# Kernel tuning notes

Measured on AMD Instinct MI355X. Metric: run time of the kernel, lower is better.

## Reference

```python
import jax, jax.numpy as jnp
import numpy as np

HEADS = 12
IDX = 0


def setup_inputs() -> dict:
    key = jax.random.key(0)
    ks = jax.random.split(key, 6)
    B, H, W, C = 16, 64, 64, 384
    x = jax.random.normal(ks[0], (B, H * W, C), dtype=jnp.float32)
    qkv_w = jax.random.normal(ks[1], (3 * C, C), dtype=jnp.float32) * 0.02
    proj_w = jax.random.normal(ks[2], (C, C), dtype=jnp.float32) * 0.02
    proj_b = jax.random.normal(ks[3], (C,), dtype=jnp.float32) * 0.02
    lepe_w = jax.random.normal(ks[4], (C, 1, 3, 3), dtype=jnp.float32) * 0.02  # depthwise, torch OIHW with I=1
    lepe_b = jax.random.normal(ks[5], (C,), dtype=jnp.float32) * 0.02
    return {"x": x, "qkv_w": qkv_w, "proj_w": proj_w, "proj_b": proj_b,
            "lepe_w": lepe_w, "lepe_b": lepe_b, "H": H, "W": W}


def _lepe_forward(x, qkv_w, proj_w, proj_b, lepe_w, lepe_b, H, W):
    B, N, C = x.shape
    hd = C // HEADS
    scale = hd ** (-0.5)
    x_img = x.reshape(B, H, W, C)

    if IDX == 0:
        # vertical strips: attend over H within each column
        x_split = jnp.transpose(x_img, (0, 2, 1, 3)).reshape(B * W, H, C)
    else:
        x_split = x_img.reshape(B * H, W, C)
    S, L, _ = x_split.shape

    qkv = (x_split @ qkv_w.T).reshape(S, L, 3, HEADS, hd)
    qkv = jnp.transpose(qkv, (2, 0, 3, 1, 4))  # (3, S, heads, L, hd)
    q, k, v = qkv[0], qkv[1], qkv[2]

    attn = jnp.einsum('shld,shmd->shlm', q, k) * scale
    attn = jax.nn.softmax(attn, axis=-1)
    out = jnp.einsum('shlm,shmd->shld', attn, v)           # (S, heads, L, hd)
    out = jnp.transpose(out, (0, 2, 1, 3)).reshape(S, L, C)
    # faithful to torch: view(B, out_H, out_W, C).view(B, H*W, C) -- no permute back for idx==0
    out_flat = out.reshape(B, H * W, C)

    # depthwise 3x3 conv LePE on the original (H, W) layout
    lepe = jax.lax.conv_general_dilated(
        jnp.transpose(x_img, (0, 3, 1, 2)), lepe_w,
        window_strides=(1, 1), padding='SAME',
        feature_group_count=C,
        dimension_numbers=('NCHW', 'OIHW', 'NCHW'))
    lepe = lepe + lepe_b[None, :, None, None]
    lepe = jnp.transpose(lepe, (0, 2, 3, 1)).reshape(B, H * W, C)

    return (out_flat + lepe) @ proj_w.T + proj_b


def reference(x, qkv_w, proj_w, proj_b, lepe_w, lepe_b, H, W):
    return _lepe_forward(x, qkv_w, proj_w, proj_b, lepe_w, lepe_b, H, W)
```

## Files before the change

### kernel.cpp

```cpp
#include <hip/hip_runtime.h>


typedef _Float16 f16;
typedef _Float16 f16x8 __attribute__((ext_vector_type(8)));
typedef float    f32x4 __attribute__((ext_vector_type(4)));

__device__ __forceinline__ f32x4 mfma_16x16x32(f16x8 a, f16x8 b, f32x4 c) {
  return __builtin_amdgcn_mfma_f32_16x16x32_f16(a, b, c, 0, 0, 0);
}

__device__ __forceinline__ void gl_lds16(const f16* g, f16* l) {
  __builtin_amdgcn_global_load_lds((const __attribute__((address_space(1))) void*)g,
                                   (__attribute__((address_space(3))) void*)l, 16, 0, 0);
}

__global__ __launch_bounds__(256) void k_cvt(const float* __restrict__ src,
                                             f16* __restrict__ dst, int n8) {
  int i = blockIdx.x * 256 + threadIdx.x;
  if (i >= n8) return;
  const f32x4* s4 = (const f32x4*)src;
  f32x4 a = s4[2 * i], b = s4[2 * i + 1];
  f16x8 o;
#pragma unroll
  for (int j = 0; j < 4; ++j) { o[j] = (f16)a[j]; o[4 + j] = (f16)b[j]; }
  *(f16x8*)&dst[(long)i * 8] = o;
}

__global__ __launch_bounds__(256) void k_prep(const float* __restrict__ x,
                                              const float* __restrict__ lw,
                                              const float* __restrict__ lb,
                                              f16* __restrict__ x16,
                                              f16* __restrict__ lepe16) {
  __shared__ float ws[9 * 384];
  __shared__ float bs[384];
  for (int i = threadIdx.x; i < 3456; i += 256) {
    int c = i / 9, tap = i - c * 9;
    ws[tap * 384 + (c & 7) * 48 + (c >> 3)] = lw[i];
  }
  for (int i = threadIdx.x; i < 384; i += 256)
    bs[(i & 7) * 48 + (i >> 3)] = lb[i];
  __syncthreads();

  int chunk = blockIdx.x * 256 + threadIdx.x;
  int token = chunk / 48;
  int c0 = (chunk - token * 48) * 8;
  int cg = c0 >> 3;
  int b = token >> 12, n = token & 4095, h = n >> 6, w = n & 63;
  const float* xb = x + (long)(b << 12) * 384;

  float a8[8];
#pragma unroll
  for (int cc = 0; cc < 8; ++cc) a8[cc] = bs[cc * 48 + cg];
  f16x8 cv;
#pragma unroll
  for (int ky = 0; ky < 3; ++ky) {
    int hh = h + ky - 1;
    if (hh < 0 || hh > 63) continue;
#pragma unroll
    for (int kx = 0; kx < 3; ++kx) {
      int ww = w + kx - 1;
      if (ww < 0 || ww > 63) continue;
      const float* p = xb + (long)((hh << 6) + ww) * 384 + c0;
      float4 u = *(const float4*)p;
      float4 v = *(const float4*)(p + 4);
      float xs[8] = {u.x, u.y, u.z, u.w, v.x, v.y, v.z, v.w};
      if (ky == 1 && kx == 1) {
#pragma unroll
        for (int cc = 0; cc < 8; ++cc) cv[cc] = (f16)xs[cc];
      }
      int tap = ky * 3 + kx;
#pragma unroll
      for (int cc = 0; cc < 8; ++cc)
        a8[cc] += xs[cc] * ws[tap * 384 + cc * 48 + cg];
    }
  }
  f16x8 o;
#pragma unroll
  for (int cc = 0; cc < 8; ++cc) o[cc] = (f16)a8[cc];
  *(f16x8*)&x16[(long)token * 384 + c0] = cv;
  *(f16x8*)&lepe16[(long)token * 384 + c0] = o;
}

__global__ __launch_bounds__(256) void k_qkv(const f16* __restrict__ A,
                                             const f16* __restrict__ Bt,
                                             f16* __restrict__ C) {
  __shared__ alignas(16) f16 smem[2 * 128 * 64];
  f16* As = smem;
  f16* Bs = smem + 128 * 64;
  f16* buf = smem;
  const int tid = threadIdx.x;
  const int lane = tid & 63;
  const int wave = tid >> 6;
  const int wr = wave >> 1, wc = wave & 1;
  const int ln = lane & 15, quad = lane >> 4;
  const int bid = blockIdx.x;
  const int xcd = bid & 7;
  const int s = bid >> 3;
  const int mq = s / 9;
  const int mt = xcd * 64 + mq;
  const int nt = s - mq * 9;
  const long m0 = (long)mt * 128;
  const int n0 = nt * 128;

  f32x4 acc[4][4] = {};
  for (int k0 = 0; k0 < 384; k0 += 64) {
#pragma unroll
    for (int r = 0; r < 4; ++r) {
      int flat = r * 256 + tid;
      int row = flat >> 3, c8 = flat & 7;
      int sc8 = (c8 ^ (row & 7)) * 8;
      gl_lds16(&A[(m0 + row) * 384 + k0 + sc8], &As[flat * 8]);
      gl_lds16(&Bt[(long)(n0 + row) * 384 + k0 + sc8], &Bs[flat * 8]);
    }
    __syncthreads();
#pragma unroll
    for (int ks = 0; ks < 2; ++ks) {
      f16x8 a[4], b[4];
#pragma unroll
      for (int i = 0; i < 4; ++i)
        a[i] = *(const f16x8*)&As[(wr * 64 + i * 16 + ln) * 64 +
                                  ((ks * 4 + quad) ^ (ln & 7)) * 8];
#pragma unroll
      for (int j = 0; j < 4; ++j)
        b[j] = *(const f16x8*)&Bs[(wc * 64 + j * 16 + ln) * 64 +
                                  ((ks * 4 + quad) ^ (ln & 7)) * 8];
#pragma unroll
      for (int i = 0; i < 4; ++i)
#pragma unroll
        for (int j = 0; j < 4; ++j)
          acc[i][j] = mfma_16x16x32(a[i], b[j], acc[i][j]);
    }
    __syncthreads();
  }

  for (int half = 0; half < 2; ++half) {
    __syncthreads();
    if (wr == half) {
#pragma unroll
      for (int i = 0; i < 4; ++i)
#pragma unroll
        for (int j = 0; j < 4; ++j)
#pragma unroll
          for (int r = 0; r < 4; ++r)
            buf[(i * 16 + quad * 4 + r) * 136 + wc * 64 + j * 16 + ln] =
                (f16)acc[i][j][r];
    }
    __syncthreads();
#pragma unroll
    for (int it = 0; it < 4; ++it) {
      int flat = it * 256 + tid;
      int row = flat >> 4;
      int c8 = flat & 15;
      int t = (int)m0 + half * 64 + row;
      int nn = t & 4095;
      long prow = (long)(t & ~4095) + ((nn & 63) << 6) + (nn >> 6);
      *(f16x8*)&C[prow * 1152 + n0 + c8 * 8] =
          *(const f16x8*)&buf[row * 136 + c8 * 8];
    }
  }
}

__global__ __launch_bounds__(256) void k_attn(const f16* __restrict__ qkv,
                                              f16* __restrict__ attnout) {
  __shared__ alignas(16) f16 shp[4][7424];
  const int lane = threadIdx.x & 63;
  const int wave = threadIdx.x >> 6;
  const int ln = lane & 15, quad = lane >> 4, q8 = quad * 8;
  const int b = blockIdx.x >> 6, w = blockIdx.x & 63;
  const long sbase = (long)b * 4096 + (long)w * 64;

  f16* qs = shp[wave];
  f16* ks = shp[wave] + 2560;
  f16* vt = shp[wave] + 5120;
  f16* ps = shp[wave];
  f16* obuf = shp[wave];
  const float qscale = 0.17677669529663687f;

  for (int hi = 0; hi < 3; ++hi) {
    const int hh = wave * 3 + hi;
#pragma unroll
    for (int r = 0; r < 4; ++r) {
      int flat = r * 64 + lane;
      int l = flat >> 2, dg = (flat & 3) * 8;
      long ta = (sbase + l) * 1152 + hh * 32 + dg;
      f16x8 qv = *(const f16x8*)&qkv[ta];
      f16x8 kv = *(const f16x8*)&qkv[ta + 384];
      f16x8 vv = *(const f16x8*)&qkv[ta + 768];
#pragma unroll
      for (int ii = 0; ii < 8; ++ii) qv[ii] = (f16)((float)qv[ii] * qscale);
      *(f16x8*)&qs[l * 40 + dg] = qv;
      *(f16x8*)&ks[l * 40 + dg] = kv;
#pragma unroll
      for (int ii = 0; ii < 8; ++ii) vt[(dg + ii) * 72 + l] = vv[ii];
    }
    f16x8 aq[4], bk[4];
#pragma unroll
    for (int i = 0; i < 4; ++i) aq[i] = *(const f16x8*)&qs[(i * 16 + ln) * 40 + q8];
#pragma unroll
    for (int j = 0; j < 4; ++j) bk[j] = *(const f16x8*)&ks[(j * 16 + ln) * 40 + q8];
    f32x4 sc[4][4] = {};
#pragma unroll
    for (int i = 0; i < 4; ++i)
#pragma unroll
      for (int j = 0; j < 4; ++j) sc[i][j] = mfma_16x16x32(aq[i], bk[j], sc[i][j]);

    float rs[4][4];
#pragma unroll
    for (int i = 0; i < 4; ++i)
#pragma unroll
      for (int r = 0; r < 4; ++r) {
        float m = -1e30f;
#pragma unroll
        for (int j = 0; j < 4; ++j) m = fmaxf(m, sc[i][j][r]);
#pragma unroll
        for (int off = 1; off < 16; off <<= 1) m = fmaxf(m, __shfl_xor(m, off, 64));
        float sum = 0.f;
#pragma unroll
        for (int j = 0; j < 4; ++j) {
          float p = __expf(sc[i][j][r] - m);
          sc[i][j][r] = p;
          sum += p;
        }
#pragma unroll
        for (int off = 1; off < 16; off <<= 1) sum += __shfl_xor(sum, off, 64);
        rs[i][r] = 1.0f / sum;
      }

#pragma unroll
    for (int i = 0; i < 4; ++i)
#pragma unroll
      for (int j = 0; j < 4; ++j)
#pragma unroll
        for (int r = 0; r < 4; ++r)
          ps[(i * 16 + quad * 4 + r) * 72 + j * 16 + ln] = (f16)sc[i][j][r];

    f32x4 oc[4][2] = {};
#pragma unroll
    for (int k2 = 0; k2 < 2; ++k2) {
      f16x8 ap[4], bv[2];
#pragma unroll
      for (int i = 0; i < 4; ++i)
        ap[i] = *(const f16x8*)&ps[(i * 16 + ln) * 72 + k2 * 32 + q8];
#pragma unroll
      for (int j = 0; j < 2; ++j)
        bv[j] = *(const f16x8*)&vt[(j * 16 + ln) * 72 + k2 * 32 + q8];
#pragma unroll
      for (int i = 0; i < 4; ++i)
#pragma unroll
        for (int j = 0; j < 2; ++j) oc[i][j] = mfma_16x16x32(ap[i], bv[j], oc[i][j]);
    }

#pragma unroll
    for (int i = 0; i < 4; ++i)
#pragma unroll
      for (int j = 0; j < 2; ++j)
#pragma unroll
        for (int r = 0; r < 4; ++r)
          obuf[(i * 16 + quad * 4 + r) * 40 + j * 16 + ln] =
              (f16)(oc[i][j][r] * rs[i][r]);
    {
      int row = lane >> 1, hf = lane & 1;
#pragma unroll
      for (int rr = 0; rr < 2; ++rr) {
        int rw = rr * 32 + row;
        const f16* ob = &obuf[rw * 40 + hf * 16];
        f16x8 o0 = *(const f16x8*)ob;
        f16x8 o1 = *(const f16x8*)(ob + 8);
        f16* gp = attnout + (sbase + rw) * 384 + hh * 32 + hf * 16;
        *(f16x8*)gp = o0;
        *(f16x8*)(gp + 8) = o1;
      }
    }
  }
}

__global__ __launch_bounds__(256) void k_proj(const f16* __restrict__ A1,
                                              const f16* __restrict__ A2,
                                              const f16* __restrict__ Bt,
                                              const float* __restrict__ bias,
                                              float* __restrict__ Cf) {
  __shared__ alignas(16) f16 smem[2 * 128 * 64];
  f16* As = smem;
  f16* Bs = smem + 128 * 64;
  float* buff = (float*)smem;
  const int tid = threadIdx.x;
  const int lane = tid & 63;
  const int wave = tid >> 6;
  const int wr = wave >> 1, wc = wave & 1;
  const int ln = lane & 15, quad = lane >> 4;
  const int bid = blockIdx.x;
  const int xcd = bid & 7;
  const int s = bid >> 3;
  const int mq = s / 3;
  const int mt = xcd * 64 + mq;
  const int nt = s - mq * 3;
  const long m0 = (long)mt * 128;
  const int n0 = nt * 128;

  f32x4 acc[4][4] = {};
  for (int k0 = 0; k0 < 384; k0 += 64) {
#pragma unroll
    for (int r = 0; r < 4; ++r) {
      int flat = r * 256 + tid;
      int row = flat >> 3, c8 = flat & 7;
      int sc8 = (c8 ^ (row & 7)) * 8;
      long ai = (m0 + row) * 384 + k0 + sc8;
      f16x8 s2 = *(const f16x8*)&A1[ai] + *(const f16x8*)&A2[ai];
      *(f16x8*)&As[flat * 8] = s2;
      gl_lds16(&Bt[(long)(n0 + row) * 384 + k0 + sc8], &Bs[flat * 8]);
    }
    __syncthreads();
#pragma unroll
    for (int ks = 0; ks < 2; ++ks) {
      f16x8 a[4], b[4];
#pragma unroll
      for (int i = 0; i < 4; ++i)
        a[i] = *(const f16x8*)&As[(wr * 64 + i * 16 + ln) * 64 +
                                  ((ks * 4 + quad) ^ (ln & 7)) * 8];
#pragma unroll
      for (int j = 0; j < 4; ++j)
        b[j] = *(const f16x8*)&Bs[(wc * 64 + j * 16 + ln) * 64 +
                                  ((ks * 4 + quad) ^ (ln & 7)) * 8];
#pragma unroll
      for (int i = 0; i < 4; ++i)
#pragma unroll
        for (int j = 0; j < 4; ++j)
          acc[i][j] = mfma_16x16x32(a[i], b[j], acc[i][j]);
    }
    __syncthreads();
  }

#pragma unroll
  for (int p = 0; p < 4; ++p) {
    __syncthreads();
    if (wr == (p >> 1)) {
      const int ib = (p & 1) * 2;
#pragma unroll
      for (int ii = 0; ii < 2; ++ii)
#pragma unroll
        for (int j = 0; j < 4; ++j)
#pragma unroll
          for (int r = 0; r < 4; ++r)
            buff[(ii * 16 + quad * 4 + r) * 132 + wc * 64 + j * 16 + ln] =
                acc[ib + ii][j][r];
    }
    __syncthreads();
#pragma unroll
    for (int it = 0; it < 4; ++it) {
      int flat = it * 256 + tid;
      int row = flat >> 5;
      int c4 = flat & 31;
      long gr = m0 + p * 32 + row;
      int col = n0 + c4 * 4;
      float4 b4 = *(const float4*)&bias[col];
      float4 o = *(const float4*)&buff[row * 132 + c4 * 4];
      o.x += b4.x; o.y += b4.y; o.z += b4.z; o.w += b4.w;
      *(float4*)&Cf[gr * 384 + col] = o;
    }
  }
}

extern "C" void kernel_launch(void* const* d_in, const int* in_sizes, int n_in,
                              void* d_out, int out_size, void* d_ws, size_t ws_size,
                              hipStream_t stream) {
  const float* x = (const float*)d_in[0];
  const float* qkv_w = (const float*)d_in[1];
  const float* proj_w = (const float*)d_in[2];
  const float* proj_b = (const float*)d_in[3];
  const float* lepe_w = (const float*)d_in[4];
  const float* lepe_b = (const float*)d_in[5];
  float* out = (float*)d_out;

  char* ws = (char*)d_ws;
  f16* w16 = (f16*)(ws + 0);
  f16* pw16 = (f16*)(ws + 884736);
  f16* x16 = (f16*)(ws + 1179648);
  f16* attnout = x16;
  f16* lepe16 = (f16*)(ws + 51511296);
  f16* qkv16 = (f16*)(ws + 101842944);

  k_cvt<<<216, 256, 0, stream>>>(qkv_w, w16, 55296);
  k_cvt<<<72, 256, 0, stream>>>(proj_w, pw16, 18432);
  k_prep<<<12288, 256, 0, stream>>>(x, lepe_w, lepe_b, x16, lepe16);
  k_qkv<<<512 * 9, 256, 0, stream>>>(x16, w16, qkv16);
  k_attn<<<1024, 256, 0, stream>>>(qkv16, attnout);
  k_proj<<<512 * 3, 256, 0, stream>>>(attnout, lepe16, pw16, proj_b, out);
}
```

Before: 459.9 us.

## Double-buffer QKV GEMM loads and enlarge tile to 256x128 with 512 threads

The QKV projection GEMM now prefetches the next K-slice into a second LDS buffer while computing on the current one, so each iteration needs only one barrier and global-to-LDS latency overlaps MFMA work. The block tile grows from 128x128 to 256x128 with 8 waves, which halves B-matrix reloads per output and halves the block count. The cost is 96KB of shared memory per block, which limits occupancy to fewer blocks per CU, and a two-pass epilogue through LDS.

```diff
diff --git a/kernel.cpp b/kernel.cpp
--- a/kernel.cpp
+++ b/kernel.cpp
@@ -81,13 +81,11 @@
   *(f16x8*)&lepe16[(long)token * 384 + c0] = o;
 }
 
-__global__ __launch_bounds__(256) void k_qkv(const f16* __restrict__ A,
+__global__ __launch_bounds__(512) void k_qkv(const f16* __restrict__ A,
                                              const f16* __restrict__ Bt,
                                              f16* __restrict__ C) {
-  __shared__ alignas(16) f16 smem[2 * 128 * 64];
-  f16* As = smem;
-  f16* Bs = smem + 128 * 64;
-  f16* buf = smem;
+  __shared__ alignas(16) f16 smem[49152];
+  f16* ebuf = smem;
   const int tid = threadIdx.x;
   const int lane = tid & 63;
   const int wave = tid >> 6;
@@ -97,32 +95,48 @@
   const int xcd = bid & 7;
   const int s = bid >> 3;
   const int mq = s / 9;
-  const int mt = xcd * 64 + mq;
+  const int mt = xcd * 32 + mq;
   const int nt = s - mq * 9;
-  const long m0 = (long)mt * 128;
+  const long m0 = (long)mt * 256;
   const int n0 = nt * 128;
 
-  f32x4 acc[4][4] = {};
-  for (int k0 = 0; k0 < 384; k0 += 64) {
+  auto stage = [&](int buf, int k0) {
+    f16* Asb = smem + buf * 16384;
+    f16* Bsb = smem + 32768 + buf * 8192;
 #pragma unroll
     for (int r = 0; r < 4; ++r) {
-      int flat = r * 256 + tid;
+      int flat = r * 512 + tid;
       int row = flat >> 3, c8 = flat & 7;
       int sc8 = (c8 ^ (row & 7)) * 8;
-      gl_lds16(&A[(m0 + row) * 384 + k0 + sc8], &As[flat * 8]);
-      gl_lds16(&Bt[(long)(n0 + row) * 384 + k0 + sc8], &Bs[flat * 8]);
-    }
-    __syncthreads();
+      gl_lds16(&A[(m0 + row) * 384 + k0 + sc8], &Asb[flat * 8]);
+    }
+#pragma unroll
+    for (int r = 0; r < 2; ++r) {
+      int flat = r * 512 + tid;
+      int row = flat >> 3, c8 = flat & 7;
+      int sc8 = (c8 ^ (row & 7)) * 8;
+      gl_lds16(&Bt[(long)(n0 + row) * 384 + k0 + sc8], &Bsb[flat * 8]);
+    }
+  };
+
+  f32x4 acc[4][4] = {};
+  stage(0, 0);
+  __syncthreads();
+  int cur = 0;
+  for (int t = 0; t < 6; ++t) {
+    if (t < 5) stage(cur ^ 1, (t + 1) * 64);
+    const f16* Ac = smem + cur * 16384;
+    const f16* Bc = smem + 32768 + cur * 8192;
 #pragma unroll
     for (int ks = 0; ks < 2; ++ks) {
       f16x8 a[4], b[4];
 #pragma unroll
       for (int i = 0; i < 4; ++i)
-        a[i] = *(const f16x8*)&As[(wr * 64 + i * 16 + ln) * 64 +
+        a[i] = *(const f16x8*)&Ac[(wr * 64 + i * 16 + ln) * 64 +
                                   ((ks * 4 + quad) ^ (ln & 7)) * 8];
 #pragma unroll
       for (int j = 0; j < 4; ++j)
-        b[j] = *(const f16x8*)&Bs[(wc * 64 + j * 16 + ln) * 64 +
+        b[j] = *(const f16x8*)&Bc[(wc * 64 + j * 16 + ln) * 64 +
                                   ((ks * 4 + quad) ^ (ln & 7)) * 8];
 #pragma unroll
       for (int i = 0; i < 4; ++i)
@@ -131,32 +145,34 @@
           acc[i][j] = mfma_16x16x32(a[i], b[j], acc[i][j]);
     }
     __syncthreads();
-  }
-
-  for (int half = 0; half < 2; ++half) {
-    __syncthreads();
-    if (wr == half) {
+    cur ^= 1;
+  }
+
+  for (int p = 0; p < 2; ++p) {
+    if ((wr >> 1) == p) {
+      const int lr0 = (wr & 1) * 64;
 #pragma unroll
       for (int i = 0; i < 4; ++i)
 #pragma unroll
         for (int j = 0; j < 4; ++j)
 #pragma unroll
           for (int r = 0; r < 4; ++r)
-            buf[(i * 16 + quad * 4 + r) * 136 + wc * 64 + j * 16 + ln] =
+            ebuf[(lr0 + i * 16 + quad * 4 + r) * 136 + wc * 64 + j * 16 + ln] =
                 (f16)acc[i][j][r];
     }
     __syncthreads();
 #pragma unroll
     for (int it = 0; it < 4; ++it) {
-      int flat = it * 256 + tid;
+      int flat = it * 512 + tid;
       int row = flat >> 4;
       int c8 = flat & 15;
-      int t = (int)m0 + half * 64 + row;
+      int t = (int)m0 + p * 128 + row;
       int nn = t & 4095;
       long prow = (long)(t & ~4095) + ((nn & 63) << 6) + (nn >> 6);
       *(f16x8*)&C[prow * 1152 + n0 + c8 * 8] =
-          *(const f16x8*)&buf[row * 136 + c8 * 8];
-    }
+          *(const f16x8*)&ebuf[row * 136 + c8 * 8];
+    }
+    __syncthreads();
   }
 }
 
@@ -382,7 +398,7 @@
   k_cvt<<<216, 256, 0, stream>>>(qkv_w, w16, 55296);
   k_cvt<<<72, 256, 0, stream>>>(proj_w, pw16, 18432);
   k_prep<<<12288, 256, 0, stream>>>(x, lepe_w, lepe_b, x16, lepe16);
-  k_qkv<<<512 * 9, 256, 0, stream>>>(x16, w16, qkv16);
+  k_qkv<<<2304, 512, 0, stream>>>(x16, w16, qkv16);
   k_attn<<<1024, 256, 0, stream>>>(qkv16, attnout);
   k_proj<<<512 * 3, 256, 0, stream>>>(attnout, lepe16, pw16, proj_b, out);
 }
```

After: 456.9 us. No clear change (-0.7%).
